# Performance work log

Hardware: AMD Instinct MI355X
Metric: run time of the kernel (lower is better)

## Reference

```python
import jax, jax.numpy as jnp
import numpy as np

S = 4096      # packed sequence length
DIM = 1024    # model dim
H = 8         # num heads
HD = 64       # per-branch head dim (head_dim // 2 in the module)
LAMBDA_INIT = 0.8 - 0.6 * float(np.exp(-0.3 * 0.0))  # depth=0 -> 0.2
EPS = 1e-5


def setup_inputs() -> dict:
    key = jax.random.key(0)
    ks = jax.random.split(key, 10)
    P = 2 * H * HD  # = 1024
    return {
        "x": jax.random.normal(ks[0], (S, DIM), jnp.float32),
        "mask": jnp.ones((1, 1, S, S), jnp.bool_),
        "Wq": jax.random.normal(ks[1], (DIM, P), jnp.float32) * 0.02,
        "Wk": jax.random.normal(ks[2], (DIM, P), jnp.float32) * 0.02,
        "Wv": jax.random.normal(ks[3], (DIM, P), jnp.float32) * 0.02,
        "Wo": jax.random.normal(ks[4], (P, DIM), jnp.float32) * 0.02,
        "lambda_q1": jax.random.normal(ks[5], (HD,), jnp.float32) * 0.1,
        "lambda_k1": jax.random.normal(ks[6], (HD,), jnp.float32) * 0.1,
        "lambda_q2": jax.random.normal(ks[7], (HD,), jnp.float32) * 0.1,
        "lambda_k2": jax.random.normal(ks[8], (HD,), jnp.float32) * 0.1,
        "subln_weight": jnp.ones((2 * HD,), jnp.float32),
    }


def reference(x, mask, Wq, Wk, Wv, Wo, lambda_q1, lambda_k1, lambda_q2,
              lambda_k2, subln_weight):
    # projections: (S, 2H, HD) split into branch index along a new axis
    xq = (x @ Wq).reshape(S, H, 2, HD)   # [2*H] view -> (H,2) contiguous split
    xk = (x @ Wk).reshape(S, H, 2, HD)
    xv = (x @ Wv).reshape(S, H, 2 * HD)
    q1, q2 = xq[:, :, 0], xq[:, :, 1]    # (S,H,HD)
    k1, k2 = xk[:, :, 0], xk[:, :, 1]

    scale = 1.0 / jnp.sqrt(jnp.float32(HD))
    bias = jnp.where(mask[0, 0], 0.0, -jnp.inf)  # (S,S) additive mask

    def sdpa(q, k):
        # q,k: (S,H,HD); xv: (S,H,2HD)
        scores = jnp.einsum('shd,thd->hst', q, k) * scale + bias  # (H,S,S)
        p = jax.nn.softmax(scores, axis=-1)
        return jnp.einsum('hst,thd->shd', p, xv)                  # (S,H,2HD)

    attn1 = sdpa(q1, k1)
    attn2 = sdpa(q2, k2)

    lam1 = jnp.exp(jnp.sum(lambda_q1 * lambda_k1))
    lam2 = jnp.exp(jnp.sum(lambda_q2 * lambda_k2))
    lambda_full = lam1 - lam2 + LAMBDA_INIT

    attn = attn1 - lambda_full * attn2                            # (S,H,2HD)
    # RMSNorm over last dim (2*HD) with learnable weight
    attn = attn * jax.lax.rsqrt(jnp.mean(attn * attn, axis=-1, keepdims=True) + EPS)
    attn = attn * subln_weight
    attn = attn * (1.0 - LAMBDA_INIT)
    return attn.reshape(S, H * 2 * HD) @ Wo                       # (S, DIM)
```

## Files before the change

### kernel.cpp

```cpp
#include <hip/hip_runtime.h>
#include <hip/hip_bf16.h>
#include <type_traits>
#include <utility>


using bf16 = __hip_bfloat16;

static constexpr int SQ = 4096;
static constexpr int DM = 1024;
static constexpr float LAMB_INIT = 0.2f;
static constexpr float KSC = 0.18033688011112043f;

typedef float  f32x4    __attribute__((ext_vector_type(4)));
typedef short  s16x4    __attribute__((ext_vector_type(4)));
typedef short  bf16x8_i __attribute__((ext_vector_type(8)));
typedef __bf16 bf16x8_b __attribute__((ext_vector_type(8)));

template<typename T, typename = void> struct mfma_ok : std::false_type {};
template<typename T> struct mfma_ok<T, std::void_t<decltype(
    __builtin_amdgcn_mfma_f32_16x16x32_bf16(std::declval<T>(), std::declval<T>(),
                                            std::declval<f32x4>(), 0, 0, 0))>>
    : std::true_type {};
using abfrag = std::conditional_t<mfma_ok<bf16x8_b>::value, bf16x8_b, bf16x8_i>;

__device__ __forceinline__ f32x4 mfma16(abfrag a, abfrag b, f32x4 c) {
    return __builtin_amdgcn_mfma_f32_16x16x32_bf16(a, b, c, 0, 0, 0);
}
__device__ __forceinline__ abfrag ldfrag(const bf16* p) {
    return *reinterpret_cast<const abfrag*>(p);
}
__device__ __forceinline__ short bf2s(bf16 b) {
    short s; __builtin_memcpy(&s, &b, 2); return s;
}
__device__ __forceinline__ float fexp2(float x) {
#if __has_builtin(__builtin_amdgcn_exp2f)
    return __builtin_amdgcn_exp2f(x);
#else
    return exp2f(x);
#endif
}
__device__ __forceinline__ int cvtpk(float lo, float hi) {
    int r;
    asm("v_cvt_pk_bf16_f32 %0, %1, %2" : "=v"(r) : "v"(lo), "v"(hi));
    return r;
}
__device__ __forceinline__ void gld_lds16(const bf16* g, bf16* l) {
    __builtin_amdgcn_global_load_lds((__attribute__((address_space(1))) void*)g,
                                     (__attribute__((address_space(3))) void*)l,
                                     16, 0, 0);
}


__global__ __launch_bounds__(256) void convert_x(const float* __restrict__ in,
                                                 bf16* __restrict__ outp)
{
    const size_t i = ((size_t)blockIdx.x * 256 + threadIdx.x) * 4;
    const f32x4 v = *reinterpret_cast<const f32x4*>(in + i);
    s16x4 o;
#pragma unroll
    for (int j = 0; j < 4; ++j) o[j] = bf2s(__float2bfloat16(v[j]));
    *reinterpret_cast<s16x4*>(outp + i) = o;
}

__global__ __launch_bounds__(256) void transpose_w(
    const float* __restrict__ Wq, const float* __restrict__ Wk,
    const float* __restrict__ Wv, const float* __restrict__ Wo,
    bf16* __restrict__ Wqt, bf16* __restrict__ Wkt,
    bf16* __restrict__ Wvt, bf16* __restrict__ Wot)
{
    const int z = blockIdx.z;
    const float* src = (z == 0) ? Wq : (z == 1) ? Wk : (z == 2) ? Wv : Wo;
    bf16* dst        = (z == 0) ? Wqt : (z == 1) ? Wkt : (z == 2) ? Wvt : Wot;
    const float scale = (z == 0) ? KSC : 1.0f;
    __shared__ float tbuf[32][33];
    const int k0 = blockIdx.x * 32, n0 = blockIdx.y * 32;
    const int c = threadIdx.x & 31, r0 = threadIdx.x >> 5;
#pragma unroll
    for (int i = 0; i < 4; ++i)
        tbuf[r0 + i * 8][c] = src[(size_t)(k0 + r0 + i * 8) * 1024 + n0 + c];
    __syncthreads();
#pragma unroll
    for (int i = 0; i < 4; ++i)
        dst[(size_t)(n0 + r0 + i * 8) * 1024 + k0 + c] =
            __float2bfloat16(tbuf[c][r0 + i * 8] * scale);
}

__global__ void lambda_kernel(const float* lq1, const float* lk1,
                              const float* lq2, const float* lk2, float* outp)
{
    const int lane = threadIdx.x;
    float a = lq1[lane] * lk1[lane];
    float b = lq2[lane] * lk2[lane];
#pragma unroll
    for (int m = 1; m < 64; m <<= 1) {
        a += __shfl_xor(a, m, 64);
        b += __shfl_xor(b, m, 64);
    }
    if (lane == 0) outp[0] = __expf(a) - __expf(b) + LAMB_INIT;
}


template<bool BF16OUT>
__device__ __forceinline__ void gemm_core(const bf16* __restrict__ A,
                                          const bf16* __restrict__ Bt,
                                          void* __restrict__ Cout,
                                          int m0, int n0, int ldc,
                                          bool vt_out, bf16* __restrict__ VT)
{
    __shared__ __align__(16) bf16 As[128 * 32];
    __shared__ __align__(16) bf16 Bs[128 * 32];
    const int tid  = threadIdx.x;
    const int wid  = tid >> 6;
    const int lane = tid & 63;
    const int l15  = lane & 15;
    const int l4   = lane >> 4;
    const int wr   = wid >> 1;
    const int wc   = wid & 1;

    const f32x4 zero4 = {0.f, 0.f, 0.f, 0.f};
    f32x4 acc[4][4];
#pragma unroll
    for (int i = 0; i < 4; ++i)
#pragma unroll
        for (int j = 0; j < 4; ++j) acc[i][j] = zero4;

    for (int kt = 0; kt < 1024; kt += 32) {
        __syncthreads();
#pragma unroll
        for (int it = 0; it < 2; ++it) {
            const int flat = it * 256 + tid;
            const int row  = flat >> 2;
            const int c16  = flat & 3;
            const int ldst = (it * 256 + wid * 64) * 8;
            gld_lds16(&A [(size_t)(m0 + row) * 1024 + kt + c16 * 8], &As[ldst]);
            gld_lds16(&Bt[(size_t)(n0 + row) * 1024 + kt + c16 * 8], &Bs[ldst]);
        }
        __syncthreads();
        abfrag a[4], b[4];
#pragma unroll
        for (int mi = 0; mi < 4; ++mi)
            a[mi] = ldfrag(&As[(wr * 64 + mi * 16 + l15) * 32 + l4 * 8]);
#pragma unroll
        for (int ni = 0; ni < 4; ++ni)
            b[ni] = ldfrag(&Bs[(wc * 64 + ni * 16 + l15) * 32 + l4 * 8]);
#pragma unroll
        for (int mi = 0; mi < 4; ++mi)
#pragma unroll
            for (int ni = 0; ni < 4; ++ni)
                acc[mi][ni] = mfma16(a[mi], b[ni], acc[mi][ni]);
    }

    if constexpr (BF16OUT) {
        if (vt_out) {
            __shared__ __align__(16) bf16 tb[32][136];
#pragma unroll
            for (int ch = 0; ch < 4; ++ch) {
                if (wc == (ch >> 1)) {
#pragma unroll
                    for (int nn = 0; nn < 2; ++nn) {
                        const int ni  = (ch & 1) * 2 + nn;
                        const int c32 = nn * 16 + l15;
#pragma unroll
                        for (int mi = 0; mi < 4; ++mi) {
                            const int rl = wr * 64 + mi * 16 + l4 * 4;
                            *(int*)&tb[c32][rl] =
                                cvtpk(acc[mi][ni][0], acc[mi][ni][1]);
                            *(int*)&tb[c32][rl + 2] =
                                cvtpk(acc[mi][ni][2], acc[mi][ni][3]);
                        }
                    }
                }
                __syncthreads();
                {
                    const int d  = tid >> 3;
                    const int pp = tid & 7;
                    const bf16* src = &tb[d][pp * 16];
                    bf16* dst = VT + (size_t)(n0 + ch * 32 + d) * SQ + m0 + pp * 16;
                    *(f32x4*)(dst)     = *(const f32x4*)(src);
                    *(f32x4*)(dst + 8) = *(const f32x4*)(src + 8);
                }
                __syncthreads();
            }
            return;
        }
    }

#pragma unroll
    for (int mi = 0; mi < 4; ++mi)
#pragma unroll
        for (int ni = 0; ni < 4; ++ni)
#pragma unroll
            for (int r = 0; r < 4; ++r) {
                const int row = m0 + wr * 64 + mi * 16 + l4 * 4 + r;
                const int col = n0 + wc * 64 + ni * 16 + l15;
                if constexpr (BF16OUT)
                    ((bf16*)Cout)[(size_t)row * ldc + col] = __float2bfloat16(acc[mi][ni][r]);
                else
                    ((float*)Cout)[(size_t)row * ldc + col] = acc[mi][ni][r];
            }
}

__global__ __launch_bounds__(256, 3) void gemm_qkv(
    const bf16* __restrict__ xbf,
    const bf16* __restrict__ Wqt, const bf16* __restrict__ Wkt,
    const bf16* __restrict__ Wvt,
    bf16* __restrict__ Qo, bf16* __restrict__ Ko, bf16* __restrict__ Vto)
{
    const int which = blockIdx.y >> 3;
    const int m0 = blockIdx.x * 128, n0 = (blockIdx.y & 7) * 128;
    if (which == 2) {
        gemm_core<true>(xbf, Wvt, nullptr, m0, n0, 1024, true, Vto);
    } else {
        const bf16* Bt = (which == 0) ? Wqt : Wkt;
        bf16* Cp       = (which == 0) ? Qo  : Ko;
        gemm_core<true>(xbf, Bt, Cp, m0, n0, 1024, false, nullptr);
    }
}

__global__ __launch_bounds__(256, 3) void gemm_out(
    const bf16* __restrict__ Amat, const bf16* __restrict__ Wot,
    float* __restrict__ out)
{
    gemm_core<false>(Amat, Wot, out, blockIdx.x * 128, blockIdx.y * 128, 1024,
                     false, nullptr);
}


__global__ __launch_bounds__(512, 2) void flash_diff(
    const bf16* __restrict__ Qm, const bf16* __restrict__ Km,
    const bf16* __restrict__ Vtm, const float* __restrict__ lam_ptr,
    const float* __restrict__ subln, bf16* __restrict__ Amat)
{
    const int bid  = blockIdx.x;
    const int h    = bid & 7;
    const int qt   = bid >> 3;
    const int tid  = threadIdx.x;
    const int wid  = tid >> 6;
    const int lane = tid & 63;
    const int l15  = lane & 15;
    const int l4   = lane >> 4;
    const int qbase = qt * 128 + wid * 16;
    const int swz   = (l15 & 7) << 4;

    constexpr int KOFF = 0, VOFF = 49152, BUFSZ = 16384;

    __shared__ __align__(16) char smem[98304];

    abfrag qf[2][2];
#pragma unroll
    for (int c = 0; c < 2; ++c)
#pragma unroll
        for (int kc = 0; kc < 2; ++kc)
            qf[c][kc] = ldfrag(&Qm[(size_t)(qbase + l15) * DM +
                                   h * 128 + c * 64 + kc * 32 + l4 * 8]);
    asm volatile("" :: "v"(qf[0][0]), "v"(qf[0][1]), "v"(qf[1][0]), "v"(qf[1][1]));

    union { abfrag f; short s[8]; } uon;
#pragma unroll
    for (int i = 0; i < 8; ++i) uon.s[i] = (short)0x3F80;
    const abfrag ones = uon.f;

    const bf16* kap[2];
    const bf16* vap[2];
#pragma unroll
    for (int it = 0; it < 2; ++it) {
        const int slot = it * 512 + tid;
        const int krow = slot >> 4;
        const int kcb  = ((slot & 15) << 4) ^ ((krow & 7) << 4);
        kap[it] = Km + (size_t)krow * DM + h * 128 + (kcb >> 1);
        const int vrow = slot >> 3;
        const int vcb  = ((slot & 7) << 4) ^ ((vrow & 7) << 4);
        vap[it] = Vtm + (size_t)(h * 128 + vrow) * SQ + (vcb >> 1);
    }
    auto stage = [&](int buf) {
        char* kd = smem + KOFF + buf * BUFSZ;
        char* vd = smem + VOFF + buf * BUFSZ;
#pragma unroll
        for (int it = 0; it < 2; ++it) {
            gld_lds16(kap[it], (bf16*)(kd + (it * 512 + wid * 64) * 16));
            kap[it] += 64 * DM;
            gld_lds16(vap[it], (bf16*)(vd + (it * 512 + wid * 64) * 16));
            vap[it] += 64;
        }
    };

    const int kLane0 = l15 * 256 + ((l4 * 16) ^ swz);
    const int kLane1 = l15 * 256 + ((64 + l4 * 16) ^ swz);
    int vLane[4];
#pragma unroll
    for (int ch = 0; ch < 2; ++ch)
#pragma unroll
        for (int hh = 0; hh < 2; ++hh)
            vLane[ch * 2 + hh] = l15 * 128 + ((ch * 64 + hh * 32 + l4 * 8) ^ swz);

    const f32x4 zero4 = {0.f, 0.f, 0.f, 0.f};
    f32x4 o_[2][8];
#pragma unroll
    for (int c = 0; c < 2; ++c)
#pragma unroll
        for (int vt = 0; vt < 8; ++vt) o_[c][vt] = zero4;
    f32x4 lacc[2] = {zero4, zero4};

    stage(0);
    stage(1);
    asm volatile("s_waitcnt vmcnt(4)" ::: "memory");
    __builtin_amdgcn_s_barrier();

    int cur = 0, nxt = 2;
    constexpr int NT = SQ / 64;
#pragma unroll 1
    for (int t = 0; t < NT; ++t) {
        const bool pf = (t + 2 < NT);
        if (pf) stage(nxt);

        const char* kbuf = smem + KOFF + cur * BUFSZ;
        const char* vbuf = smem + VOFF + cur * BUFSZ;
        const char* kb0  = kbuf + kLane0;
        const char* kb1  = kbuf + kLane1;

        abfrag pa[2][2];
#pragma unroll
        for (int c = 0; c < 2; ++c) {
            f32x4 sc[4];
#pragma unroll
            for (int j = 0; j < 4; ++j) {
                const abfrag k0 = *(const abfrag*)(kb0 + (j * 4096 + c * 128));
                const abfrag k1 = *(const abfrag*)(kb1 + (j * 4096 + c * 128));
                f32x4 z = mfma16(k0, qf[c][0], zero4);
                sc[j] = mfma16(k1, qf[c][1], z);
            }
            f32x4 pe[4];
#pragma unroll
            for (int j = 0; j < 4; ++j)
#pragma unroll
                for (int r = 0; r < 4; ++r) pe[j][r] = fexp2(sc[j][r]);
            union { abfrag f; int i[4]; } u0, u1;
            u0.i[0] = cvtpk(pe[0][0], pe[0][1]);
            u0.i[1] = cvtpk(pe[0][2], pe[0][3]);
            u0.i[2] = cvtpk(pe[1][0], pe[1][1]);
            u0.i[3] = cvtpk(pe[1][2], pe[1][3]);
            u1.i[0] = cvtpk(pe[2][0], pe[2][1]);
            u1.i[1] = cvtpk(pe[2][2], pe[2][3]);
            u1.i[2] = cvtpk(pe[3][0], pe[3][1]);
            u1.i[3] = cvtpk(pe[3][2], pe[3][3]);
            pa[c][0] = u0.f;
            pa[c][1] = u1.f;
        }

        const char* vb00 = vbuf + vLane[0];
        const char* vb01 = vbuf + vLane[1];
        const char* vb10 = vbuf + vLane[2];
        const char* vb11 = vbuf + vLane[3];

        __builtin_amdgcn_s_setprio(1);
        lacc[0] = mfma16(pa[0][0], ones, lacc[0]);
        lacc[0] = mfma16(pa[0][1], ones, lacc[0]);
        lacc[1] = mfma16(pa[1][0], ones, lacc[1]);
        lacc[1] = mfma16(pa[1][1], ones, lacc[1]);
#pragma unroll
        for (int vt = 0; vt < 8; ++vt) {
            union { abfrag f; s16x4 hh[2]; } v0, v1;
            v0.hh[0] = *(const s16x4*)(vb00 + vt * 2048);
            v0.hh[1] = *(const s16x4*)(vb01 + vt * 2048);
            v1.hh[0] = *(const s16x4*)(vb10 + vt * 2048);
            v1.hh[1] = *(const s16x4*)(vb11 + vt * 2048);
            o_[0][vt] = mfma16(pa[0][0], v0.f, o_[0][vt]);
            o_[1][vt] = mfma16(pa[1][0], v0.f, o_[1][vt]);
            o_[0][vt] = mfma16(pa[0][1], v1.f, o_[0][vt]);
            o_[1][vt] = mfma16(pa[1][1], v1.f, o_[1][vt]);
        }
        __builtin_amdgcn_s_setprio(0);

        if (pf) asm volatile("s_waitcnt vmcnt(4)" ::: "memory");
        else    asm volatile("s_waitcnt vmcnt(0)" ::: "memory");
        __builtin_amdgcn_s_barrier();
        cur = (cur == 2) ? 0 : cur + 1;
        nxt = (nxt == 2) ? 0 : nxt + 1;
    }

    const float lam = lam_ptr[0];
    float il1[4], il2[4];
#pragma unroll
    for (int r = 0; r < 4; ++r) {
        il1[r] = 1.f / lacc[0][r];
        il2[r] = lam / lacc[1][r];
    }
#pragma unroll
    for (int r = 0; r < 4; ++r) {
        float comb[8];
        float ss = 0.f;
#pragma unroll
        for (int vt = 0; vt < 8; ++vt) {
            const float v = o_[0][vt][r] * il1[r] - o_[1][vt][r] * il2[r];
            comb[vt] = v;
            ss += v * v;
        }
        ss += __shfl_xor(ss, 1, 64);
        ss += __shfl_xor(ss, 2, 64);
        ss += __shfl_xor(ss, 4, 64);
        ss += __shfl_xor(ss, 8, 64);
        const float rinv = rsqrtf(ss * (1.f / 128.f) + 1e-5f);
        const int row = qbase + l4 * 4 + r;
#pragma unroll
        for (int vt = 0; vt < 8; ++vt) {
            const float outv = comb[vt] * rinv * subln[vt * 16 + l15] * 0.8f;
            Amat[(size_t)row * DM + h * 128 + vt * 16 + l15] = __float2bfloat16(outv);
        }
    }
}


extern "C" void kernel_launch(void* const* d_in, const int* in_sizes, int n_in,
                              void* d_out, int out_size, void* d_ws, size_t ws_size,
                              hipStream_t stream)
{
    (void)in_sizes; (void)n_in; (void)out_size; (void)ws_size;
    const float* x    = (const float*)d_in[0];
    const float* Wq   = (const float*)d_in[2];
    const float* Wk   = (const float*)d_in[3];
    const float* Wv   = (const float*)d_in[4];
    const float* Wo   = (const float*)d_in[5];
    const float* lq1  = (const float*)d_in[6];
    const float* lk1  = (const float*)d_in[7];
    const float* lq2  = (const float*)d_in[8];
    const float* lk2  = (const float*)d_in[9];
    const float* subw = (const float*)d_in[10];

    char* ws = (char*)d_ws;
    size_t off = 0;
    auto take = [&](size_t n) { void* p = ws + off; off += (n + 255) & ~(size_t)255; return p; };
    bf16* xbf = (bf16*)take((size_t)SQ * DM * 2);
    bf16* Wqt = (bf16*)take((size_t)DM * DM * 2);
    bf16* Wkt = (bf16*)take((size_t)DM * DM * 2);
    bf16* Wvt = (bf16*)take((size_t)DM * DM * 2);
    bf16* Wot = (bf16*)take((size_t)DM * DM * 2);
    bf16* Qb  = (bf16*)take((size_t)SQ * DM * 2);
    bf16* Kb  = (bf16*)take((size_t)SQ * DM * 2);
    bf16* Vtb = (bf16*)take((size_t)SQ * DM * 2);
    bf16* Am  = (bf16*)take((size_t)SQ * DM * 2);
    float* lamp = (float*)take(256);

    convert_x   <<<dim3(SQ * DM / 1024), dim3(256), 0, stream>>>(x, xbf);
    transpose_w <<<dim3(32, 32, 4),      dim3(256), 0, stream>>>(Wq, Wk, Wv, Wo, Wqt, Wkt, Wvt, Wot);
    lambda_kernel<<<dim3(1),             dim3(64),  0, stream>>>(lq1, lk1, lq2, lk2, lamp);
    gemm_qkv    <<<dim3(32, 24),         dim3(256), 0, stream>>>(xbf, Wqt, Wkt, Wvt, Qb, Kb, Vtb);
    flash_diff  <<<dim3(256),            dim3(512), 0, stream>>>(Qb, Kb, Vtb, lamp, subw, Am);
    gemm_out    <<<dim3(32, 8),          dim3(256), 0, stream>>>(Am, Wot, (float*)d_out);
}
```

Before: 186.5 us.

## Double GEMM K-tile to 64 and XOR-swizzle LDS layout to avoid bank conflicts

The projection GEMM core now stages 64-wide K slices instead of 32, which halves the number of barrier pairs per K loop, and runs two MFMA halves per stage. The LDS tiles use an XOR swizzle on 16-byte chunks keyed by row so that fragment reads across the 128-byte rows do not conflict on banks. This doubles LDS use per block and adds address arithmetic, which could lower occupancy.

```diff
diff --git a/kernel.cpp b/kernel.cpp
--- a/kernel.cpp
+++ b/kernel.cpp
@@ -107,8 +107,8 @@
                                           int m0, int n0, int ldc,
                                           bool vt_out, bf16* __restrict__ VT)
 {
-    __shared__ __align__(16) bf16 As[128 * 32];
-    __shared__ __align__(16) bf16 Bs[128 * 32];
+    __shared__ __align__(16) bf16 As[128 * 64];
+    __shared__ __align__(16) bf16 Bs[128 * 64];
     const int tid  = threadIdx.x;
     const int wid  = tid >> 6;
     const int lane = tid & 63;
@@ -117,6 +117,14 @@
     const int wr   = wid >> 1;
     const int wc   = wid & 1;
 
+    int srow[4], scb[4];
+#pragma unroll
+    for (int it = 0; it < 4; ++it) {
+        const int slot = it * 256 + tid;
+        srow[it] = slot >> 3;
+        scb[it]  = ((slot & 7) << 4) ^ ((srow[it] & 7) << 4);
+    }
+
     const f32x4 zero4 = {0.f, 0.f, 0.f, 0.f};
     f32x4 acc[4][4];
 #pragma unroll
@@ -124,30 +132,38 @@
 #pragma unroll
         for (int j = 0; j < 4; ++j) acc[i][j] = zero4;
 
-    for (int kt = 0; kt < 1024; kt += 32) {
+    for (int kt = 0; kt < 1024; kt += 64) {
         __syncthreads();
 #pragma unroll
-        for (int it = 0; it < 2; ++it) {
-            const int flat = it * 256 + tid;
-            const int row  = flat >> 2;
-            const int c16  = flat & 3;
+        for (int it = 0; it < 4; ++it) {
             const int ldst = (it * 256 + wid * 64) * 8;
-            gld_lds16(&A [(size_t)(m0 + row) * 1024 + kt + c16 * 8], &As[ldst]);
-            gld_lds16(&Bt[(size_t)(n0 + row) * 1024 + kt + c16 * 8], &Bs[ldst]);
+            gld_lds16(&A [(size_t)(m0 + srow[it]) * 1024 + kt + (scb[it] >> 1)],
+                      &As[ldst]);
+            gld_lds16(&Bt[(size_t)(n0 + srow[it]) * 1024 + kt + (scb[it] >> 1)],
+                      &Bs[ldst]);
         }
         __syncthreads();
-        abfrag a[4], b[4];
-#pragma unroll
-        for (int mi = 0; mi < 4; ++mi)
-            a[mi] = ldfrag(&As[(wr * 64 + mi * 16 + l15) * 32 + l4 * 8]);
-#pragma unroll
-        for (int ni = 0; ni < 4; ++ni)
-            b[ni] = ldfrag(&Bs[(wc * 64 + ni * 16 + l15) * 32 + l4 * 8]);
-#pragma unroll
-        for (int mi = 0; mi < 4; ++mi)
-#pragma unroll
-            for (int ni = 0; ni < 4; ++ni)
-                acc[mi][ni] = mfma16(a[mi], b[ni], acc[mi][ni]);
+#pragma unroll
+        for (int half = 0; half < 2; ++half) {
+            abfrag a[4], b[4];
+#pragma unroll
+            for (int mi = 0; mi < 4; ++mi) {
+                const int row = wr * 64 + mi * 16 + l15;
+                a[mi] = *(const abfrag*)((const char*)As + row * 128 +
+                          ((half * 64 + l4 * 16) ^ ((row & 7) << 4)));
+            }
+#pragma unroll
+            for (int ni = 0; ni < 4; ++ni) {
+                const int row = wc * 64 + ni * 16 + l15;
+                b[ni] = *(const abfrag*)((const char*)Bs + row * 128 +
+                          ((half * 64 + l4 * 16) ^ ((row & 7) << 4)));
+            }
+#pragma unroll
+            for (int mi = 0; mi < 4; ++mi)
+#pragma unroll
+                for (int ni = 0; ni < 4; ++ni)
+                    acc[mi][ni] = mfma16(a[mi], b[ni], acc[mi][ni]);
+        }
     }
 
     if constexpr (BF16OUT) {
```

Result: faster. 177.1 us (-5.1%).
